# Kernel tuning notes

Measured on AMD Instinct MI355X. Metric: run time of the kernel, lower is better.

The kernel has to match this reference:

```python
import jax, jax.numpy as jnp
import numpy as np

G = 2            # num codevector groups
C = 320          # codes per group
VQ_DIM = 256     # codevector_dim
D = VQ_DIM // G  # per-group code dim = 128
TAU = 2.0        # gumbel temperature


def setup_inputs() -> dict:
    key = jax.random.key(0)
    k1, k2, k3, k4, k5, k6 = jax.random.split(key, 6)
    B, T, H = 16, 3072, 512
    x = jax.random.normal(k1, (B, T, H), dtype=jnp.float32)
    masked_token_idx = jax.random.randint(k2, (B, T), 0, 2) > 0  # bool mask
    gumbel_noise = jax.random.gumbel(k3, (B * T * G, C), dtype=jnp.float32)
    q_proj_w = jax.random.normal(k4, (G * C, H), dtype=jnp.float32) * (1.0 / np.sqrt(H))
    q_proj_b = jax.random.normal(k5, (G * C,), dtype=jnp.float32) * 0.02
    codevectors = jax.random.uniform(k6, (1, G * C, D), dtype=jnp.float32)
    return {"x": x, "masked_token_idx": masked_token_idx, "gumbel_noise": gumbel_noise,
            "q_proj_w": q_proj_w, "q_proj_b": q_proj_b, "codevectors": codevectors}


def _perplexity(probs, mask_flat):
    # probs: [B*T, G, C]; masked mean over tokens, then per-codebook perplexity
    m = mask_flat.astype(probs.dtype)
    denom = jnp.maximum(m.sum(), 1.0)
    p = jnp.einsum('ngc,n->gc', probs, m) / denom  # [G, C]
    perp_per_cb = jnp.exp(-jnp.sum(p * jnp.log(p + 1e-7), axis=-1))
    return perp_per_cb.sum()


def reference(x, masked_token_idx, gumbel_noise, q_proj_w, q_proj_b, codevectors):
    B, T, H = x.shape
    N = B * T
    logits = jnp.einsum('bth,kh->btk', x, q_proj_w) + q_proj_b  # [B,T,G*C]
    l = logits.reshape(N * G, C)
    # hard gumbel-softmax with straight-through estimator (training path)
    y_soft = jax.nn.softmax((l + gumbel_noise) / TAU, axis=-1)
    idx = jnp.argmax(y_soft, axis=-1)
    y_hard = jax.nn.one_hot(idx, C, dtype=y_soft.dtype)
    codevector_probs = y_hard + y_soft - jax.lax.stop_gradient(y_soft)  # [N*G, C]
    # perplexity from plain (non-tempered) softmax of logits, over masked tokens
    soft = jax.nn.softmax(l.reshape(N, G, C), axis=-1)
    perplexity = _perplexity(soft, masked_token_idx.reshape(-1))
    # codevector gather-multiply-sum, expressed as a grouped contraction
    # (same math as probs.unsqueeze(-1)*codevectors then sum over codes)
    cv = codevectors.reshape(G, C, D)
    probs3 = codevector_probs.reshape(N, G, C)
    selected = jnp.einsum('ngc,gcd->ngd', probs3, cv).reshape(B, T, G * D)
    return selected, perplexity
```

## Files before the change

### kernel.cpp

```cpp
#include <hip/hip_runtime.h>
#include <hip/hip_bf16.h>
#include <math.h>

#define TOKS 49152
#define HD   512
#define GN   2
#define CN   320
#define DN   128
#define BM   128
#define NTHR 512
#define LSTR 324

#define BH_OFF 0
#define BL_OFF 20480
#define AH_OFF 40960
#define AL_OFF 49152
#define SBUF   57344
#define SMEM_DYN (2 * SBUF)
#define PSUM_OFF 82944

#define BMF  32
#define NTHRF 256
#define WSTR 33

#define WS_WELEMS ((size_t)(GN * CN) * HD)
#define WS_W_OFF  4096
#define WS_MID    (WS_W_OFF + 4 * WS_WELEMS)

typedef _Float16 f16x8 __attribute__((ext_vector_type(8)));
typedef float    fx4   __attribute__((ext_vector_type(4)));

#define GLD_LDS16(gp, lp)                                                    \
  __builtin_amdgcn_global_load_lds(                                          \
      (const __attribute__((address_space(1))) void*)(gp),                   \
      (__attribute__((address_space(3))) void*)(lp), 16, 0, 0)

__global__ void k_zero(float* pp) {
  int t = threadIdx.x;
  if (t < GN * CN) pp[t] = 0.f;
}

__global__ __launch_bounds__(256) void k_split(const float* __restrict__ src,
                                               _Float16* __restrict__ dh,
                                               _Float16* __restrict__ dl,
                                               float* __restrict__ pp) {
  if (blockIdx.x < 3) {
    int i = blockIdx.x * 256 + threadIdx.x;
    if (i < GN * CN) pp[i] = 0.f;
  }
  size_t t    = (size_t)blockIdx.x * 256 + threadIdx.x;
  int    lane = (int)(t & 63);
  size_t blob = t >> 6;
  int    k0   = (int)(blob & 15);
  size_t rb   = blob >> 4;
  const float* p = src + (rb * 16 + (lane & 15)) * HD + k0 * 32 + (lane >> 4) * 8;
  fx4 u = *(const fx4*)p;
  fx4 v = *(const fx4*)(p + 4);
  f16x8 h8, l8;
  #pragma unroll
  for (int e = 0; e < 4; ++e) {
    _Float16 hu = (_Float16)u[e], hv = (_Float16)v[e];
    h8[e]     = hu;
    h8[e + 4] = hv;
    l8[e]     = (_Float16)((u[e] - (float)hu) * 512.f);
    l8[e + 4] = (_Float16)((v[e] - (float)hv) * 512.f);
  }
  *(f16x8*)(dh + t * 8) = h8;
  *(f16x8*)(dl + t * 8) = l8;
}

__global__ __launch_bounds__(NTHR, 2) void k_gemm_ep(
    const float* __restrict__ x, const int* __restrict__ mask,
    const float* __restrict__ gnoise, const float* __restrict__ bias,
    const float* __restrict__ cv, const _Float16* __restrict__ wh,
    const _Float16* __restrict__ wl, float* __restrict__ out,
    float* __restrict__ pp)
{
  extern __shared__ __align__(16) char smem[];
  float* lg   = (float*)smem;
  float* psum = (float*)(smem + PSUM_OFF);

  const int u   = blockIdx.x;
  const int mt  = ((u >> 4) << 3) | (u & 7);
  const int g   = (u >> 3) & 1;
  const int m0  = mt * BM;
  const int tid = threadIdx.x;
  const int tc  = tid & 63;
  const int w   = tid >> 6;
  const int wr  = w >> 2;
  const int wc  = w & 3;
  const int l15 = tid & 15;
  const int l4  = tc >> 4;

  fx4 aH[4][5], aL[4][5];
  #pragma unroll
  for (int rf = 0; rf < 4; ++rf)
    #pragma unroll
    for (int cf = 0; cf < 5; ++cf) {
      aH[rf][cf] = (fx4){0.f, 0.f, 0.f, 0.f};
      aL[rf][cf] = (fx4){0.f, 0.f, 0.f, 0.f};
    }

  const _Float16* bb = (w < 4) ? wh : wl;
  const int cb0      = (w < 4) ? w * 5 : w * 5 - 20;
  const _Float16* bsrc = bb + (size_t)(g * 20 + cb0) * 8192 + (size_t)tc * 8;
  const float* asrc = x + (size_t)(m0 + w * 16 + (tc & 15)) * HD + (tc >> 4) * 8;
  const int aslot = w * 1024 + tc * 16;

  fx4 au, av;

#define STAGE_A_LOAD(T) do {                                                 \
    au = *(const fx4*)(asrc + (size_t)(T) * 32);                             \
    av = *(const fx4*)(asrc + (size_t)(T) * 32 + 4);                         \
  } while (0)

#define STAGE_B(T, BASE) do {                                                \
    _Pragma("unroll")                                                        \
    for (int q = 0; q < 5; ++q)                                              \
      GLD_LDS16(bsrc + (size_t)q * 8192 + (size_t)(T) * 512,                 \
                (BASE) + w * 5120 + q * 1024);                               \
  } while (0)

#define STAGE_A_WRITE(BASE) do {                                             \
    f16x8 h8, l8;                                                            \
    _Pragma("unroll")                                                        \
    for (int e = 0; e < 4; ++e) {                                            \
      _Float16 hh;                                                           \
      hh = (_Float16)au[e]; h8[e] = hh;                                      \
      l8[e] = (_Float16)((au[e] - (float)hh) * 512.f);                       \
      hh = (_Float16)av[e]; h8[e + 4] = hh;                                  \
      l8[e + 4] = (_Float16)((av[e] - (float)hh) * 512.f);                   \
    }                                                                        \
    *(f16x8*)((BASE) + AH_OFF + aslot) = h8;                                 \
    *(f16x8*)((BASE) + AL_OFF + aslot) = l8;                                 \
  } while (0)

#define COMPUTE(BASE) do {                                                   \
    f16x8 Ah0 = *(const f16x8*)((BASE) + AH_OFF + (wr * 4 + 0) * 1024 + tc * 16); \
    f16x8 Ah1 = *(const f16x8*)((BASE) + AH_OFF + (wr * 4 + 1) * 1024 + tc * 16); \
    f16x8 Ah2 = *(const f16x8*)((BASE) + AH_OFF + (wr * 4 + 2) * 1024 + tc * 16); \
    f16x8 Ah3 = *(const f16x8*)((BASE) + AH_OFF + (wr * 4 + 3) * 1024 + tc * 16); \
    f16x8 Al0 = *(const f16x8*)((BASE) + AL_OFF + (wr * 4 + 0) * 1024 + tc * 16); \
    f16x8 Al1 = *(const f16x8*)((BASE) + AL_OFF + (wr * 4 + 1) * 1024 + tc * 16); \
    f16x8 Al2 = *(const f16x8*)((BASE) + AL_OFF + (wr * 4 + 2) * 1024 + tc * 16); \
    f16x8 Al3 = *(const f16x8*)((BASE) + AL_OFF + (wr * 4 + 3) * 1024 + tc * 16); \
    _Pragma("unroll")                                                        \
    for (int cf = 0; cf < 5; ++cf) {                                         \
      f16x8 Bh = *(const f16x8*)((BASE) + BH_OFF + (wc * 5 + cf) * 1024 + tc * 16); \
      f16x8 Bl = *(const f16x8*)((BASE) + BL_OFF + (wc * 5 + cf) * 1024 + tc * 16); \
      aH[0][cf] = __builtin_amdgcn_mfma_f32_16x16x32_f16(Ah0, Bh, aH[0][cf], 0, 0, 0); \
      aH[1][cf] = __builtin_amdgcn_mfma_f32_16x16x32_f16(Ah1, Bh, aH[1][cf], 0, 0, 0); \
      aH[2][cf] = __builtin_amdgcn_mfma_f32_16x16x32_f16(Ah2, Bh, aH[2][cf], 0, 0, 0); \
      aH[3][cf] = __builtin_amdgcn_mfma_f32_16x16x32_f16(Ah3, Bh, aH[3][cf], 0, 0, 0); \
      aL[0][cf] = __builtin_amdgcn_mfma_f32_16x16x32_f16(Ah0, Bl, aL[0][cf], 0, 0, 0); \
      aL[0][cf] = __builtin_amdgcn_mfma_f32_16x16x32_f16(Al0, Bh, aL[0][cf], 0, 0, 0); \
      aL[1][cf] = __builtin_amdgcn_mfma_f32_16x16x32_f16(Ah1, Bl, aL[1][cf], 0, 0, 0); \
      aL[1][cf] = __builtin_amdgcn_mfma_f32_16x16x32_f16(Al1, Bh, aL[1][cf], 0, 0, 0); \
      aL[2][cf] = __builtin_amdgcn_mfma_f32_16x16x32_f16(Ah2, Bl, aL[2][cf], 0, 0, 0); \
      aL[2][cf] = __builtin_amdgcn_mfma_f32_16x16x32_f16(Al2, Bh, aL[2][cf], 0, 0, 0); \
      aL[3][cf] = __builtin_amdgcn_mfma_f32_16x16x32_f16(Ah3, Bl, aL[3][cf], 0, 0, 0); \
      aL[3][cf] = __builtin_amdgcn_mfma_f32_16x16x32_f16(Al3, Bh, aL[3][cf], 0, 0, 0); \
    }                                                                        \
  } while (0)

  STAGE_A_LOAD(0);
  STAGE_B(0, smem);
  STAGE_A_WRITE(smem);
  __syncthreads();
  #pragma unroll 2
  for (int t = 0; t < 16; ++t) {
    char* cur = smem + (size_t)(t & 1) * SBUF;
    char* nxt = smem + (size_t)((t & 1) ^ 1) * SBUF;
    if (t < 15) { STAGE_A_LOAD(t + 1); STAGE_B(t + 1, nxt); }
    COMPUTE(cur);
    if (t < 15) STAGE_A_WRITE(nxt);
    __syncthreads();
  }
#undef STAGE_A_LOAD
#undef STAGE_B
#undef STAGE_A_WRITE
#undef COMPUTE

  float bj[5];
  #pragma unroll
  for (int cf = 0; cf < 5; ++cf) bj[cf] = bias[g * CN + wc * 80 + cf * 16 + l15];

  float pacc[5] = {0.f, 0.f, 0.f, 0.f, 0.f};
  #pragma unroll
  for (int p = 0; p < 2; ++p) {
    if (wr == p) {
      #pragma unroll
      for (int cf = 0; cf < 5; ++cf) {
        const int col = wc * 80 + cf * 16 + l15;
        #pragma unroll
        for (int rf = 0; rf < 4; ++rf)
          #pragma unroll
          for (int e = 0; e < 4; ++e)
            lg[(rf * 16 + l4 * 4 + e) * LSTR + col] =
                aH[rf][cf][e] + aL[rf][cf][e] * (1.f / 512.f) + bj[cf];
      }
    }
    __syncthreads();
    #pragma unroll
    for (int i = 0; i < 8; ++i) {
      const int rl = w * 8 + i;
      const int n  = m0 + p * 64 + rl;
      const size_t grow = ((size_t)n * GN + g) * CN;
      float lv[5], gv[5];
      #pragma unroll
      for (int j = 0; j < 5; ++j) lv[j] = lg[rl * LSTR + tc + 64 * j];
      #pragma unroll
      for (int j = 0; j < 5; ++j) gv[j] = gnoise[grow + tc + 64 * j];

      float bv = -3.4e38f; int bi = 1 << 30;
      #pragma unroll
      for (int j = 0; j < 5; ++j) {
        float v = lv[j] + gv[j];
        if (v > bv) { bv = v; bi = tc + 64 * j; }
      }
      for (int off = 1; off < 64; off <<= 1) {
        float ov = __shfl_xor(bv, off);
        int   oi = __shfl_xor(bi, off);
        if (ov > bv || (ov == bv && oi < bi)) { bv = ov; bi = oi; }
      }

      float mx = lv[0];
      #pragma unroll
      for (int j = 1; j < 5; ++j) mx = fmaxf(mx, lv[j]);
      for (int off = 1; off < 64; off <<= 1) mx = fmaxf(mx, __shfl_xor(mx, off));
      float e[5], s = 0.f;
      #pragma unroll
      for (int j = 0; j < 5; ++j) { e[j] = __expf(lv[j] - mx); s += e[j]; }
      for (int off = 1; off < 64; off <<= 1) s += __shfl_xor(s, off);
      const float inv = 1.f / s;
      const float mlt = (mask[n] != 0) ? 1.f : 0.f;
      #pragma unroll
      for (int j = 0; j < 5; ++j) pacc[j] += mlt * e[j] * inv;

      const float2* cvr = (const float2*)(cv + ((size_t)(g * CN + bi)) * DN);
      float2* o2 = (float2*)(out + (size_t)n * (GN * DN) + g * DN);
      o2[tc] = cvr[tc];
    }
    __syncthreads();
  }

  #pragma unroll
  for (int j = 0; j < 5; ++j) psum[w * CN + tc + 64 * j] = pacc[j];
  __syncthreads();
  for (int c = tid; c < CN; c += NTHR) {
    float s = 0.f;
    #pragma unroll
    for (int q = 0; q < 8; ++q) s += psum[q * CN + c];
    atomicAdd(&pp[g * CN + c], s);
  }
}

__global__ __launch_bounds__(NTHRF) void k_main_fp32(
    const float* __restrict__ x, const int* __restrict__ mask,
    const float* __restrict__ gnoise, const float* __restrict__ W,
    const float* __restrict__ bias, const float* __restrict__ cv,
    float* __restrict__ out, float* __restrict__ pp)
{
  __shared__ __align__(16) char fsmem[47360];
  float* w_lds = (float*)fsmem;
  float* xs    = (float*)(fsmem + 42240);
  float* lgf   = (float*)fsmem;
  float* psum  = (float*)(fsmem + 42240);

  const int m0  = blockIdx.x * BMF;
  const int g   = blockIdx.y;
  const int tid = threadIdx.x;
  const int tc  = tid & 63;
  const int tr  = tid >> 6;
  const int r0  = tr * 8;

  float acc[8][5];
  #pragma unroll
  for (int i = 0; i < 8; ++i)
    #pragma unroll
    for (int j = 0; j < 5; ++j) acc[i][j] = 0.f;

  const float* Wg = W + (size_t)g * CN * HD;

  for (int k0 = 0; k0 < HD; k0 += 32) {
    __syncthreads();
    #pragma unroll
    for (int t = 0; t < 10; ++t) {
      int idx = tid + t * NTHRF;
      int c   = idx >> 3;
      int k4  = idx & 7;
      float4 wv4 = *(const float4*)(Wg + (size_t)c * HD + k0 + k4 * 4);
      float* dst = &w_lds[c * WSTR + k4 * 4];
      dst[0] = wv4.x; dst[1] = wv4.y; dst[2] = wv4.z; dst[3] = wv4.w;
    }
    {
      int r = tid >> 3, k4 = tid & 7;
      float4 xv = *(const float4*)(x + (size_t)(m0 + r) * HD + k0 + k4 * 4);
      float* dst = &xs[r * 32 + k4 * 4];
      dst[0] = xv.x; dst[1] = xv.y; dst[2] = xv.z; dst[3] = xv.w;
    }
    __syncthreads();
    #pragma unroll
    for (int kk = 0; kk < 32; kk += 4) {
      float xq[8][4];
      #pragma unroll
      for (int i = 0; i < 8; ++i) {
        float4 t4 = *(const float4*)&xs[(r0 + i) * 32 + kk];
        xq[i][0] = t4.x; xq[i][1] = t4.y; xq[i][2] = t4.z; xq[i][3] = t4.w;
      }
      #pragma unroll
      for (int q = 0; q < 4; ++q) {
        float wv[5];
        #pragma unroll
        for (int j = 0; j < 5; ++j) wv[j] = w_lds[(tc + 64 * j) * WSTR + kk + q];
        #pragma unroll
        for (int i = 0; i < 8; ++i)
          #pragma unroll
          for (int j = 0; j < 5; ++j)
            acc[i][j] = fmaf(xq[i][q], wv[j], acc[i][j]);
      }
    }
  }
  __syncthreads();

  float bj[5];
  #pragma unroll
  for (int j = 0; j < 5; ++j) bj[j] = bias[g * CN + tc + 64 * j];
  #pragma unroll
  for (int i = 0; i < 8; ++i)
    #pragma unroll
    for (int j = 0; j < 5; ++j)
      lgf[(r0 + i) * CN + tc + 64 * j] = acc[i][j] + bj[j];
  __syncthreads();

  float pacc[5] = {0.f, 0.f, 0.f, 0.f, 0.f};
  #pragma unroll
  for (int i = 0; i < 8; ++i) {
    const int r = r0 + i;
    const int n = m0 + r;
    const size_t grow = ((size_t)n * GN + g) * CN;
    float lv[5], gv[5];
    #pragma unroll
    for (int j = 0; j < 5; ++j) lv[j] = lgf[r * CN + tc + 64 * j];
    #pragma unroll
    for (int j = 0; j < 5; ++j) gv[j] = gnoise[grow + tc + 64 * j];

    float bv = -3.4e38f; int bi = 1 << 30;
    #pragma unroll
    for (int j = 0; j < 5; ++j) {
      float v = lv[j] + gv[j];
      if (v > bv) { bv = v; bi = tc + 64 * j; }
    }
    for (int off = 1; off < 64; off <<= 1) {
      float ov = __shfl_xor(bv, off);
      int   oi = __shfl_xor(bi, off);
      if (ov > bv || (ov == bv && oi < bi)) { bv = ov; bi = oi; }
    }

    float mx = lv[0];
    #pragma unroll
    for (int j = 1; j < 5; ++j) mx = fmaxf(mx, lv[j]);
    for (int off = 1; off < 64; off <<= 1) mx = fmaxf(mx, __shfl_xor(mx, off));
    float e[5], s = 0.f;
    #pragma unroll
    for (int j = 0; j < 5; ++j) { e[j] = expf(lv[j] - mx); s += e[j]; }
    for (int off = 1; off < 64; off <<= 1) s += __shfl_xor(s, off);
    const float inv = 1.f / s;
    const float mlt = (mask[n] != 0) ? 1.f : 0.f;
    #pragma unroll
    for (int j = 0; j < 5; ++j) pacc[j] += mlt * e[j] * inv;

    const float2* cvr = (const float2*)(cv + ((size_t)(g * CN + bi)) * DN);
    float2* o2 = (float2*)(out + (size_t)n * (GN * DN) + g * DN);
    o2[tc] = cvr[tc];
  }

  #pragma unroll
  for (int j = 0; j < 5; ++j) psum[tr * CN + tc + 64 * j] = pacc[j];
  __syncthreads();
  for (int c = tid; c < CN; c += NTHRF) {
    float s = psum[c] + psum[CN + c] + psum[2 * CN + c] + psum[3 * CN + c];
    atomicAdd(&pp[g * CN + c], s);
  }
}

__global__ __launch_bounds__(640) void k_final(
    const float* __restrict__ pp, const int* __restrict__ mask,
    float* __restrict__ out, int out_off)
{
  __shared__ float red[10];
  __shared__ float eL[GN * CN];
  __shared__ float perp_parts[GN];
  const int tid = threadIdx.x;

  float cnt = 0.f;
  for (int i = tid; i < TOKS; i += 640) cnt += (mask[i] != 0) ? 1.f : 0.f;
  for (int off = 1; off < 64; off <<= 1) cnt += __shfl_xor(cnt, off);
  if ((tid & 63) == 0) red[tid >> 6] = cnt;
  __syncthreads();
  float denom = 0.f;
  #pragma unroll
  for (int w = 0; w < 10; ++w) denom += red[w];
  denom = fmaxf(denom, 1.f);

  const float p = pp[tid] / denom;
  eL[tid] = p * logf(p + 1e-7f);
  __syncthreads();

  if (tid < 2 * 64) {
    const int gg = tid >> 6, ll = tid & 63;
    float s = 0.f;
    #pragma unroll
    for (int j = 0; j < 5; ++j) s += eL[gg * CN + ll + 64 * j];
    for (int off = 1; off < 64; off <<= 1) s += __shfl_xor(s, off);
    if (ll == 0) perp_parts[gg] = expf(-s);
  }
  __syncthreads();
  if (tid == 0) out[out_off] = perp_parts[0] + perp_parts[1];
}

extern "C" void kernel_launch(void* const* d_in, const int* in_sizes, int n_in,
                              void* d_out, int out_size, void* d_ws, size_t ws_size,
                              hipStream_t stream) {
  const float* x     = (const float*)d_in[0];
  const int*   mask  = (const int*)d_in[1];
  const float* gn    = (const float*)d_in[2];
  const float* W     = (const float*)d_in[3];
  const float* bias  = (const float*)d_in[4];
  const float* cv    = (const float*)d_in[5];
  float* out = (float*)d_out;
  float* pp  = (float*)d_ws;

  if (ws_size >= WS_MID) {
    _Float16* wh = (_Float16*)((char*)d_ws + WS_W_OFF);
    _Float16* wl = wh + WS_WELEMS;
    hipLaunchKernelGGL(k_split, dim3((int)(WS_WELEMS / 8 / 256)), dim3(256), 0,
                       stream, W, wh, wl, pp);
    hipLaunchKernelGGL(k_gemm_ep, dim3(TOKS / BM * GN), dim3(NTHR), SMEM_DYN,
                       stream, x, mask, gn, bias, cv, wh, wl, out, pp);
  } else {
    hipLaunchKernelGGL(k_zero, dim3(1), dim3(640), 0, stream, pp);
    hipLaunchKernelGGL(k_main_fp32, dim3(TOKS / BMF, GN), dim3(NTHRF), 0, stream,
                       x, mask, gn, W, bias, cv, out, pp);
  }

  hipLaunchKernelGGL(k_final, dim3(1), dim3(640), 0, stream,
                     pp, mask, out, out_size - 1);
}
```

Baseline: 207.9 us.

## Use single fp16 GEMM with exact fp32 rescoring of top-3 argmax candidates

New measurement: 391.7 us. +88.5%, slower.

```diff
diff --git a/kernel.cpp b/kernel.cpp
--- a/kernel.cpp
+++ b/kernel.cpp
@@ -12,12 +12,10 @@
 #define LSTR 324
 
 #define BH_OFF 0
-#define BL_OFF 20480
-#define AH_OFF 40960
-#define AL_OFF 49152
-#define SBUF   57344
+#define AH_OFF 20480
+#define SBUF   28672
 #define SMEM_DYN (2 * SBUF)
-#define PSUM_OFF 82944
+#define PSUM_OFF 41472
 
 #define BMF  32
 #define NTHRF 256
@@ -25,7 +23,7 @@
 
 #define WS_WELEMS ((size_t)(GN * CN) * HD)
 #define WS_W_OFF  4096
-#define WS_MID    (WS_W_OFF + 4 * WS_WELEMS)
+#define WS_MID    (WS_W_OFF + 2 * WS_WELEMS)
 
 typedef _Float16 f16x8 __attribute__((ext_vector_type(8)));
 typedef float    fx4   __attribute__((ext_vector_type(4)));
@@ -42,7 +40,6 @@
 
 __global__ __launch_bounds__(256) void k_split(const float* __restrict__ src,
                                                _Float16* __restrict__ dh,
-                                               _Float16* __restrict__ dl,
                                                float* __restrict__ pp) {
   if (blockIdx.x < 3) {
     int i = blockIdx.x * 256 + threadIdx.x;
@@ -56,24 +53,20 @@
   const float* p = src + (rb * 16 + (lane & 15)) * HD + k0 * 32 + (lane >> 4) * 8;
   fx4 u = *(const fx4*)p;
   fx4 v = *(const fx4*)(p + 4);
-  f16x8 h8, l8;
+  f16x8 h8;
   #pragma unroll
   for (int e = 0; e < 4; ++e) {
-    _Float16 hu = (_Float16)u[e], hv = (_Float16)v[e];
-    h8[e]     = hu;
-    h8[e + 4] = hv;
-    l8[e]     = (_Float16)((u[e] - (float)hu) * 512.f);
-    l8[e + 4] = (_Float16)((v[e] - (float)hv) * 512.f);
+    h8[e]     = (_Float16)u[e];
+    h8[e + 4] = (_Float16)v[e];
   }
   *(f16x8*)(dh + t * 8) = h8;
-  *(f16x8*)(dl + t * 8) = l8;
-}
-
-__global__ __launch_bounds__(NTHR, 2) void k_gemm_ep(
+}
+
+__global__ __launch_bounds__(NTHR, 4) void k_gemm_ep(
     const float* __restrict__ x, const int* __restrict__ mask,
     const float* __restrict__ gnoise, const float* __restrict__ bias,
-    const float* __restrict__ cv, const _Float16* __restrict__ wh,
-    const _Float16* __restrict__ wl, float* __restrict__ out,
+    const float* __restrict__ cv, const float* __restrict__ W,
+    const _Float16* __restrict__ wh, float* __restrict__ out,
     float* __restrict__ pp)
 {
   extern __shared__ __align__(16) char smem[];
@@ -92,18 +85,14 @@
   const int l15 = tid & 15;
   const int l4  = tc >> 4;
 
-  fx4 aH[4][5], aL[4][5];
+  fx4 aH[4][5];
   #pragma unroll
   for (int rf = 0; rf < 4; ++rf)
     #pragma unroll
-    for (int cf = 0; cf < 5; ++cf) {
-      aH[rf][cf] = (fx4){0.f, 0.f, 0.f, 0.f};
-      aL[rf][cf] = (fx4){0.f, 0.f, 0.f, 0.f};
-    }
-
-  const _Float16* bb = (w < 4) ? wh : wl;
-  const int cb0      = (w < 4) ? w * 5 : w * 5 - 20;
-  const _Float16* bsrc = bb + (size_t)(g * 20 + cb0) * 8192 + (size_t)tc * 8;
+    for (int cf = 0; cf < 5; ++cf) aH[rf][cf] = (fx4){0.f, 0.f, 0.f, 0.f};
+
+  const _Float16* bsrc0 = wh + (size_t)(g * 20 + 2 * w) * 8192 + (size_t)tc * 8;
+  const _Float16* bsrcE = wh + (size_t)(g * 20 + 16 + w) * 8192 + (size_t)tc * 8;
   const float* asrc = x + (size_t)(m0 + w * 16 + (tc & 15)) * HD + (tc >> 4) * 8;
   const int aslot = w * 1024 + tc * 16;
 
@@ -115,24 +104,21 @@
   } while (0)
 
 #define STAGE_B(T, BASE) do {                                                \
-    _Pragma("unroll")                                                        \
-    for (int q = 0; q < 5; ++q)                                              \
-      GLD_LDS16(bsrc + (size_t)q * 8192 + (size_t)(T) * 512,                 \
-                (BASE) + w * 5120 + q * 1024);                               \
+    GLD_LDS16(bsrc0 + (size_t)(T) * 512, (BASE) + BH_OFF + 2 * w * 1024);    \
+    GLD_LDS16(bsrc0 + 8192 + (size_t)(T) * 512,                              \
+              (BASE) + BH_OFF + (2 * w + 1) * 1024);                         \
+    if (w < 4)                                                               \
+      GLD_LDS16(bsrcE + (size_t)(T) * 512, (BASE) + BH_OFF + (16 + w) * 1024);\
   } while (0)
 
 #define STAGE_A_WRITE(BASE) do {                                             \
-    f16x8 h8, l8;                                                            \
+    f16x8 h8;                                                                \
     _Pragma("unroll")                                                        \
     for (int e = 0; e < 4; ++e) {                                            \
-      _Float16 hh;                                                           \
-      hh = (_Float16)au[e]; h8[e] = hh;                                      \
-      l8[e] = (_Float16)((au[e] - (float)hh) * 512.f);                       \
-      hh = (_Float16)av[e]; h8[e + 4] = hh;                                  \
-      l8[e + 4] = (_Float16)((av[e] - (float)hh) * 512.f);                   \
+      h8[e]     = (_Float16)au[e];                                           \
+      h8[e + 4] = (_Float16)av[e];                                           \
     }                                                                        \
     *(f16x8*)((BASE) + AH_OFF + aslot) = h8;                                 \
-    *(f16x8*)((BASE) + AL_OFF + aslot) = l8;                                 \
   } while (0)
 
 #define COMPUTE(BASE) do {                                                   \
@@ -140,26 +126,13 @@
     f16x8 Ah1 = *(const f16x8*)((BASE) + AH_OFF + (wr * 4 + 1) * 1024 + tc * 16); \
     f16x8 Ah2 = *(const f16x8*)((BASE) + AH_OFF + (wr * 4 + 2) * 1024 + tc * 16); \
     f16x8 Ah3 = *(const f16x8*)((BASE) + AH_OFF + (wr * 4 + 3) * 1024 + tc * 16); \
-    f16x8 Al0 = *(const f16x8*)((BASE) + AL_OFF + (wr * 4 + 0) * 1024 + tc * 16); \
-    f16x8 Al1 = *(const f16x8*)((BASE) + AL_OFF + (wr * 4 + 1) * 1024 + tc * 16); \
-    f16x8 Al2 = *(const f16x8*)((BASE) + AL_OFF + (wr * 4 + 2) * 1024 + tc * 16); \
-    f16x8 Al3 = *(const f16x8*)((BASE) + AL_OFF + (wr * 4 + 3) * 1024 + tc * 16); \
     _Pragma("unroll")                                                        \
     for (int cf = 0; cf < 5; ++cf) {                                         \
       f16x8 Bh = *(const f16x8*)((BASE) + BH_OFF + (wc * 5 + cf) * 1024 + tc * 16); \
-      f16x8 Bl = *(const f16x8*)((BASE) + BL_OFF + (wc * 5 + cf) * 1024 + tc * 16); \
       aH[0][cf] = __builtin_amdgcn_mfma_f32_16x16x32_f16(Ah0, Bh, aH[0][cf], 0, 0, 0); \
       aH[1][cf] = __builtin_amdgcn_mfma_f32_16x16x32_f16(Ah1, Bh, aH[1][cf], 0, 0, 0); \
       aH[2][cf] = __builtin_amdgcn_mfma_f32_16x16x32_f16(Ah2, Bh, aH[2][cf], 0, 0, 0); \
       aH[3][cf] = __builtin_amdgcn_mfma_f32_16x16x32_f16(Ah3, Bh, aH[3][cf], 0, 0, 0); \
-      aL[0][cf] = __builtin_amdgcn_mfma_f32_16x16x32_f16(Ah0, Bl, aL[0][cf], 0, 0, 0); \
-      aL[0][cf] = __builtin_amdgcn_mfma_f32_16x16x32_f16(Al0, Bh, aL[0][cf], 0, 0, 0); \
-      aL[1][cf] = __builtin_amdgcn_mfma_f32_16x16x32_f16(Ah1, Bl, aL[1][cf], 0, 0, 0); \
-      aL[1][cf] = __builtin_amdgcn_mfma_f32_16x16x32_f16(Al1, Bh, aL[1][cf], 0, 0, 0); \
-      aL[2][cf] = __builtin_amdgcn_mfma_f32_16x16x32_f16(Ah2, Bl, aL[2][cf], 0, 0, 0); \
-      aL[2][cf] = __builtin_amdgcn_mfma_f32_16x16x32_f16(Al2, Bh, aL[2][cf], 0, 0, 0); \
-      aL[3][cf] = __builtin_amdgcn_mfma_f32_16x16x32_f16(Ah3, Bl, aL[3][cf], 0, 0, 0); \
-      aL[3][cf] = __builtin_amdgcn_mfma_f32_16x16x32_f16(Al3, Bh, aL[3][cf], 0, 0, 0); \
     }                                                                        \
   } while (0)
 
@@ -187,42 +160,72 @@
 
   float pacc[5] = {0.f, 0.f, 0.f, 0.f, 0.f};
   #pragma unroll
-  for (int p = 0; p < 2; ++p) {
-    if (wr == p) {
-      #pragma unroll
-      for (int cf = 0; cf < 5; ++cf) {
-        const int col = wc * 80 + cf * 16 + l15;
+  for (int p = 0; p < 4; ++p) {
+    if (wr == (p >> 1)) {
+      #pragma unroll
+      for (int q = 0; q < 2; ++q) {
+        const int rf = (p & 1) * 2 + q;
         #pragma unroll
-        for (int rf = 0; rf < 4; ++rf)
+        for (int cf = 0; cf < 5; ++cf) {
+          const int col = wc * 80 + cf * 16 + l15;
           #pragma unroll
           for (int e = 0; e < 4; ++e)
-            lg[(rf * 16 + l4 * 4 + e) * LSTR + col] =
-                aH[rf][cf][e] + aL[rf][cf][e] * (1.f / 512.f) + bj[cf];
+            lg[(q * 16 + l4 * 4 + e) * LSTR + col] = aH[rf][cf][e] + bj[cf];
+        }
       }
     }
     __syncthreads();
     #pragma unroll
-    for (int i = 0; i < 8; ++i) {
-      const int rl = w * 8 + i;
-      const int n  = m0 + p * 64 + rl;
+    for (int i = 0; i < 4; ++i) {
+      const int rl = w * 4 + i;
+      const int n  = m0 + p * 32 + rl;
       const size_t grow = ((size_t)n * GN + g) * CN;
-      float lv[5], gv[5];
+      float lv[5], va[5];
       #pragma unroll
       for (int j = 0; j < 5; ++j) lv[j] = lg[rl * LSTR + tc + 64 * j];
       #pragma unroll
-      for (int j = 0; j < 5; ++j) gv[j] = gnoise[grow + tc + 64 * j];
-
-      float bv = -3.4e38f; int bi = 1 << 30;
-      #pragma unroll
-      for (int j = 0; j < 5; ++j) {
-        float v = lv[j] + gv[j];
-        if (v > bv) { bv = v; bi = tc + 64 * j; }
+      for (int j = 0; j < 5; ++j) va[j] = lv[j] + gnoise[grow + tc + 64 * j];
+
+      int cand[3];
+      #pragma unroll
+      for (int c = 0; c < 3; ++c) {
+        float bv = -3.4e38f; int bi = 1 << 30;
+        #pragma unroll
+        for (int j = 0; j < 5; ++j) {
+          if (va[j] > bv) { bv = va[j]; bi = tc + 64 * j; }
+        }
+        for (int off = 1; off < 64; off <<= 1) {
+          float ov = __shfl_xor(bv, off);
+          int   oi = __shfl_xor(bi, off);
+          if (ov > bv || (ov == bv && oi < bi)) { bv = ov; bi = oi; }
+        }
+        cand[c] = bi;
+        #pragma unroll
+        for (int j = 0; j < 5; ++j)
+          if (tc + 64 * j == bi) va[j] = -3.4e38f;
       }
-      for (int off = 1; off < 64; off <<= 1) {
-        float ov = __shfl_xor(bv, off);
-        int   oi = __shfl_xor(bi, off);
-        if (ov > bv || (ov == bv && oi < bi)) { bv = ov; bi = oi; }
+
+      const fx4* xr = (const fx4*)(x + (size_t)n * HD);
+      fx4 xa = xr[tc * 2], xb = xr[tc * 2 + 1];
+      float d[3];
+      #pragma unroll
+      for (int c = 0; c < 3; ++c) {
+        const fx4* wrow = (const fx4*)(W + (size_t)(g * CN + cand[c]) * HD);
+        fx4 wa = wrow[tc * 2], wb = wrow[tc * 2 + 1];
+        float s = xa[0]*wa[0] + xa[1]*wa[1] + xa[2]*wa[2] + xa[3]*wa[3]
+                + xb[0]*wb[0] + xb[1]*wb[1] + xb[2]*wb[2] + xb[3]*wb[3];
+        for (int off = 1; off < 64; off <<= 1) s += __shfl_xor(s, off);
+        d[c] = s;
       }
+      float extra = 0.f;
+      if (tc < 3)
+        extra = gnoise[grow + cand[tc]] + bias[g * CN + cand[tc]];
+      const float t0 = d[0] + __shfl(extra, 0);
+      const float t1 = d[1] + __shfl(extra, 1);
+      const float t2 = d[2] + __shfl(extra, 2);
+      int   win = cand[0]; float wv = t0;
+      if (t1 > wv || (t1 == wv && cand[1] < win)) { wv = t1; win = cand[1]; }
+      if (t2 > wv || (t2 == wv && cand[2] < win)) { wv = t2; win = cand[2]; }
 
       float mx = lv[0];
       #pragma unroll
@@ -237,7 +240,7 @@
       #pragma unroll
       for (int j = 0; j < 5; ++j) pacc[j] += mlt * e[j] * inv;
 
-      const float2* cvr = (const float2*)(cv + ((size_t)(g * CN + bi)) * DN);
+      const float2* cvr = (const float2*)(cv + ((size_t)(g * CN + win)) * DN);
       float2* o2 = (float2*)(out + (size_t)n * (GN * DN) + g * DN);
       o2[tc] = cvr[tc];
     }
@@ -433,11 +436,10 @@
 
   if (ws_size >= WS_MID) {
     _Float16* wh = (_Float16*)((char*)d_ws + WS_W_OFF);
-    _Float16* wl = wh + WS_WELEMS;
     hipLaunchKernelGGL(k_split, dim3((int)(WS_WELEMS / 8 / 256)), dim3(256), 0,
-                       stream, W, wh, wl, pp);
+                       stream, W, wh, pp);
     hipLaunchKernelGGL(k_gemm_ep, dim3(TOKS / BM * GN), dim3(NTHR), SMEM_DYN,
-                       stream, x, mask, gn, bias, cv, wh, wl, out, pp);
+                       stream, x, mask, gn, bias, cv, W, wh, out, pp);
   } else {
     hipLaunchKernelGGL(k_zero, dim3(1), dim3(640), 0, stream, pp);
     hipLaunchKernelGGL(k_main_fp32, dim3(TOKS / BMF, GN), dim3(NTHRF), 0, stream,
```

## Deepen GEMM load pipeline with manual vmcnt waits and raw barriers

Applied to the files above, without the earlier changes.

Result: slower. 216.2 us (+4.0%).

```diff
diff --git a/kernel.cpp b/kernel.cpp
--- a/kernel.cpp
+++ b/kernel.cpp
@@ -34,6 +34,12 @@
   __builtin_amdgcn_global_load_lds(                                          \
       (const __attribute__((address_space(1))) void*)(gp),                   \
       (__attribute__((address_space(3))) void*)(lp), 16, 0, 0)
+
+#define WAITVM(N) asm volatile("s_waitcnt vmcnt(" #N ")" ::: "memory")
+#define LGKM0()   asm volatile("s_waitcnt lgkmcnt(0)" ::: "memory")
+#define RAW_BAR() do { asm volatile("" ::: "memory");                        \
+    __builtin_amdgcn_s_barrier();                                            \
+    asm volatile("" ::: "memory"); } while (0)
 
 __global__ void k_zero(float* pp) {
   int t = threadIdx.x;
@@ -109,12 +115,10 @@
 
   fx4 au, av;
 
-#define STAGE_A_LOAD(T) do {                                                 \
+#define ISSUE_AB(T, BASE) do {                                               \
     au = *(const fx4*)(asrc + (size_t)(T) * 32);                             \
     av = *(const fx4*)(asrc + (size_t)(T) * 32 + 4);                         \
-  } while (0)
-
-#define STAGE_B(T, BASE) do {                                                \
+    __builtin_amdgcn_sched_barrier(0);                                       \
     _Pragma("unroll")                                                        \
     for (int q = 0; q < 5; ++q)                                              \
       GLD_LDS16(bsrc + (size_t)q * 8192 + (size_t)(T) * 512,                 \
@@ -163,21 +167,32 @@
     }                                                                        \
   } while (0)
 
-  STAGE_A_LOAD(0);
-  STAGE_B(0, smem);
+  ISSUE_AB(0, smem);
   STAGE_A_WRITE(smem);
-  __syncthreads();
+  ISSUE_AB(1, smem + SBUF);
+  WAITVM(7);
+  LGKM0();
+  RAW_BAR();
+
   #pragma unroll 2
   for (int t = 0; t < 16; ++t) {
     char* cur = smem + (size_t)(t & 1) * SBUF;
     char* nxt = smem + (size_t)((t & 1) ^ 1) * SBUF;
-    if (t < 15) { STAGE_A_LOAD(t + 1); STAGE_B(t + 1, nxt); }
+    __builtin_amdgcn_s_setprio(1);
     COMPUTE(cur);
+    __builtin_amdgcn_s_setprio(0);
     if (t < 15) STAGE_A_WRITE(nxt);
-    __syncthreads();
-  }
-#undef STAGE_A_LOAD
-#undef STAGE_B
+    RAW_BAR();
+    if (t < 14) {
+      ISSUE_AB(t + 2, cur);
+      WAITVM(7);
+    } else {
+      WAITVM(0);
+    }
+    LGKM0();
+    RAW_BAR();
+  }
+#undef ISSUE_AB
 #undef STAGE_A_WRITE
 #undef COMPUTE
 
```
